# Kernel tuning notes

Hardware: AMD Instinct MI355X
Metric: run time of the kernel (lower is better)

The kernel has to match this reference:

```python
import jax, jax.numpy as jnp
import numpy as np

N = 100000   # nodes
E = 1600000  # edges (no self loops; module adds them)
D = 128      # in_dim == out_dim
BN_EPS = 1e-5
NORM_EPS = 1e-12


def setup_inputs() -> dict:
    key = jax.random.key(0)
    ks = jax.random.split(key, 9)
    x = jax.random.normal(ks[0], (N, D), jnp.float32)
    src = jax.random.randint(ks[1], (E,), 0, N, dtype=jnp.int32)
    dst = jax.random.randint(ks[2], (E,), 0, N, dtype=jnp.int32)
    dst = jnp.where(dst == src, (dst + 1) % N, dst)  # no pre-existing self loops
    edge_index = jnp.stack([src, dst], axis=0)
    edge_w = jax.random.uniform(ks[3], (E, 2), jnp.float32)
    # MySAGEConv.linear: Linear(2*D -> D) since concat=True
    W_lin = jax.random.normal(ks[4], (2 * D, D), jnp.float32) * (1.0 / np.sqrt(2 * D))
    b_lin = jnp.zeros((D,), jnp.float32)
    # BatchNorm1d(D)
    gamma = jnp.ones((D,), jnp.float32)
    beta = jnp.zeros((D,), jnp.float32)
    # PositionEmbedding(2, D): Linear(2->D//2, no bias), ReLU, Linear(D//2->D, no bias)
    pos_w1 = jax.random.normal(ks[5], (2, D // 2), jnp.float32) * 0.1
    pos_w2 = jax.random.normal(ks[6], (D // 2, D), jnp.float32) * 0.1
    return {"x": x, "edge_index": edge_index, "edge_w": edge_w,
            "W_lin": W_lin, "b_lin": b_lin, "gamma": gamma, "beta": beta,
            "pos_w1": pos_w1, "pos_w2": pos_w2}


def reference(x, edge_index, edge_w, W_lin, b_lin, gamma, beta, pos_w1, pos_w2):
    src, dst = edge_index[0], edge_index[1]
    # Position embedding is computed by the block but DISCARDED inside MySAGEConv.forward,
    # because add_remaining_self_loops(edge_index, None, 1, N) overwrites edge_weight with None.
    _pe = jnp.maximum(edge_w @ pos_w1, 0.0) @ pos_w2  # [E, D], unused (faithful to bug)
    # add_remaining_self_loops: append a self loop for every node
    loops = jnp.arange(N, dtype=src.dtype)
    src_f = jnp.concatenate([src, loops])
    dst_f = jnp.concatenate([dst, loops])
    # message = x_j (edge_weight is None); aggr = 'mean' scatter over destinations
    msg = x[src_f]                                           # [E+N, D] gather
    summed = jax.ops.segment_sum(msg, dst_f, num_segments=N)  # [N, D] scatter-add
    cnt = jax.ops.segment_sum(jnp.ones((E + N, 1), x.dtype), dst_f, num_segments=N)
    aggr = summed / cnt                                      # every node has >=1 (self loop)
    # update: concat + linear + L2 normalize
    h = jnp.concatenate([x, aggr], axis=-1) @ W_lin + b_lin   # [N, D]
    h = h / jnp.maximum(jnp.linalg.norm(h, axis=-1, keepdims=True), NORM_EPS)
    # BatchNorm1d (training-mode batch stats, biased variance)
    mu = jnp.mean(h, axis=0)
    var = jnp.var(h, axis=0)
    h = (h - mu) * jax.lax.rsqrt(var + BN_EPS) * gamma + beta
    # residual (in_dim == out_dim) + ReLU
    return jnp.maximum(h + x, 0.0)
```

## Files before the change

kernel.cpp:

```cpp
#include <hip/hip_runtime.h>
#include <hip/hip_bf16.h>

typedef __attribute__((ext_vector_type(4))) float f32x4;
typedef __attribute__((ext_vector_type(8))) short short8;
typedef unsigned short u16;
typedef unsigned long long u64;

#define NSLICE 64
#define LDSN 12544

static __device__ __forceinline__ u16 f2bf(float f) {
    __hip_bfloat16 h = __float2bfloat16(f);
    return __builtin_bit_cast(u16, h);
}
static __device__ __forceinline__ float bf2f(u16 u) {
    unsigned int w = ((unsigned int)u) << 16;
    return __builtin_bit_cast(float, w);
}

__global__ void k_pre(const float* __restrict__ x, u16* __restrict__ xb, int total8,
                      const int* __restrict__ dst, int* __restrict__ part,
                      int E, int chunk, int n, int cvtBlocks, int sl4) {
    __shared__ int lh[LDSN];
    int tid = threadIdx.x;
    if ((int)blockIdx.x < cvtBlocks) {
        const float4* x4 = (const float4*)x;
        int stride = cvtBlocks * 256;
        for (int i = blockIdx.x * 256 + tid; i < total8; i += stride) {
            float4 a = x4[i * 2], b = x4[i * 2 + 1];
            union { u16 u[8]; short8 v; } o;
            o.u[0] = f2bf(a.x); o.u[1] = f2bf(a.y); o.u[2] = f2bf(a.z); o.u[3] = f2bf(a.w);
            o.u[4] = f2bf(b.x); o.u[5] = f2bf(b.y); o.u[6] = f2bf(b.z); o.u[7] = f2bf(b.w);
            *(short8*)(xb + (size_t)i * 8) = o.v;
        }
    } else {
        int b = blockIdx.x - cvtBlocks;
        int g = b & 7;
        int s = b >> 3;
        int lo = g * chunk;
        int hi = min(lo + chunk, n);
        int cnt = hi - lo;
        for (int i = tid; i < cnt; i += 256) lh[i] = 0;
        __syncthreads();
        int E4 = E >> 2;
        const int4* d4 = (const int4*)dst;
        int i40 = s * sl4, i41 = min(i40 + sl4, E4);
        for (int i = i40 + tid; i < i41; i += 256) {
            int4 v = d4[i];
            if (v.x >= lo && v.x < hi) atomicAdd(&lh[v.x - lo], 1);
            if (v.y >= lo && v.y < hi) atomicAdd(&lh[v.y - lo], 1);
            if (v.z >= lo && v.z < hi) atomicAdd(&lh[v.z - lo], 1);
            if (v.w >= lo && v.w < hi) atomicAdd(&lh[v.w - lo], 1);
        }
        if (s == NSLICE - 1) {
            for (int e = E4 * 4 + tid; e < E; e += 256) {
                int d = dst[e];
                if (d >= lo && d < hi) atomicAdd(&lh[d - lo], 1);
            }
        }
        __syncthreads();
        int* pp = part + (size_t)s * n + lo;
        for (int i = tid; i < cnt; i += 256) pp[i] = lh[i];
    }
}

__global__ void k_scan_a(int* __restrict__ part, int* __restrict__ deg,
                         int* __restrict__ bsum, int n) {
    __shared__ int sm[256];
    int tid = threadIdx.x;
    int i = blockIdx.x * 256 + tid;
    int tot = 0;
    if (i < n) {
        int run = 0;
#pragma unroll
        for (int s = 0; s < NSLICE; ++s) {
            size_t idx = (size_t)s * n + i;
            int t = part[idx];
            part[idx] = run;
            run += t;
        }
        tot = run;
        deg[i] = run;
    }
    sm[tid] = tot;
    __syncthreads();
    for (int ofs = 128; ofs > 0; ofs >>= 1) {
        if (tid < ofs) sm[tid] += sm[tid + ofs];
        __syncthreads();
    }
    if (tid == 0) bsum[blockIdx.x] = sm[0];
}

__global__ void k_scan_b(const int* __restrict__ bsum, int* __restrict__ boff, int nb,
                         int* __restrict__ offN) {
    __shared__ int s[512];
    int tid = threadIdx.x;
    int v = (tid < nb) ? bsum[tid] : 0;
    s[tid] = v;
    __syncthreads();
    for (int ofs = 1; ofs < 512; ofs <<= 1) {
        int t = (tid >= ofs) ? s[tid - ofs] : 0;
        __syncthreads();
        s[tid] += t;
        __syncthreads();
    }
    if (tid < nb) boff[tid] = s[tid] - v;
    if (tid == nb - 1) offN[0] = s[tid];
}

__global__ void k_scan_c(const int* __restrict__ deg, const int* __restrict__ boff,
                         int* __restrict__ off, int n) {
    __shared__ int s[256];
    int tid = threadIdx.x;
    int i = blockIdx.x * 256 + tid;
    int v = (i < n) ? deg[i] : 0;
    s[tid] = v;
    __syncthreads();
    for (int ofs = 1; ofs < 256; ofs <<= 1) {
        int t = (tid >= ofs) ? s[tid - ofs] : 0;
        __syncthreads();
        s[tid] += t;
        __syncthreads();
    }
    int excl = s[tid] - v + boff[blockIdx.x];
    if (i < n) off[i] = excl;
}

__global__ void k_fill(const int* __restrict__ src, const int* __restrict__ dst,
                       const int* __restrict__ off, const int* __restrict__ pre,
                       int* __restrict__ csr, int E, int chunk, int n, int sl4) {
    __shared__ int lcnt[LDSN];
    int tid = threadIdx.x;
    int g = blockIdx.x & 7;
    int s = blockIdx.x >> 3;
    int lo = g * chunk;
    int hi = min(lo + chunk, n);
    int cnt = hi - lo;
    for (int i = tid; i < cnt; i += 256) lcnt[i] = 0;
    __syncthreads();
    int E4 = E >> 2;
    const int4* d4 = (const int4*)dst;
    const int4* s4 = (const int4*)src;
    const int* prs = pre + (size_t)s * n;
    int i40 = s * sl4, i41 = min(i40 + sl4, E4);
    for (int i = i40 + tid; i < i41; i += 256) {
        int4 v = d4[i];
        int4 u = s4[i];
        if (v.x >= lo && v.x < hi) {
            int p = off[v.x] + prs[v.x] + atomicAdd(&lcnt[v.x - lo], 1);
            csr[p] = u.x;
        }
        if (v.y >= lo && v.y < hi) {
            int p = off[v.y] + prs[v.y] + atomicAdd(&lcnt[v.y - lo], 1);
            csr[p] = u.y;
        }
        if (v.z >= lo && v.z < hi) {
            int p = off[v.z] + prs[v.z] + atomicAdd(&lcnt[v.z - lo], 1);
            csr[p] = u.z;
        }
        if (v.w >= lo && v.w < hi) {
            int p = off[v.w] + prs[v.w] + atomicAdd(&lcnt[v.w - lo], 1);
            csr[p] = u.w;
        }
    }
    if (s == NSLICE - 1) {
        for (int e = E4 * 4 + tid; e < E; e += 256) {
            int d = dst[e];
            if (d >= lo && d < hi) {
                int p = off[d] + prs[d] + atomicAdd(&lcnt[d - lo], 1);
                csr[p] = src[e];
            }
        }
    }
}

__global__ void k_aggr(const u16* __restrict__ xb, const int* __restrict__ off,
                       const int* __restrict__ csr, u16* __restrict__ aggr, int n) {
    int node = (blockIdx.x * blockDim.x + threadIdx.x) >> 6;
    if (node >= n) return;
    int lane = threadIdx.x & 63;
    int c = lane & 15;
    int j = lane >> 4;
    const short8* x8 = (const short8*)xb;
    int s0 = off[node], s1 = off[node + 1];
    float acc[8] = {0.f, 0.f, 0.f, 0.f, 0.f, 0.f, 0.f, 0.f};
    int e = s0;
    for (; e + 16 <= s1; e += 16) {
        int r0 = csr[e + j], r1 = csr[e + j + 4], r2 = csr[e + j + 8], r3 = csr[e + j + 12];
        short8 v0 = x8[(size_t)r0 * 16 + c];
        short8 v1 = x8[(size_t)r1 * 16 + c];
        short8 v2 = x8[(size_t)r2 * 16 + c];
        short8 v3 = x8[(size_t)r3 * 16 + c];
#pragma unroll
        for (int i = 0; i < 8; ++i)
            acc[i] += (bf2f((u16)v0[i]) + bf2f((u16)v1[i])) +
                      (bf2f((u16)v2[i]) + bf2f((u16)v3[i]));
    }
    for (int r = e + j; r < s1; r += 4) {
        short8 v = x8[(size_t)csr[r] * 16 + c];
#pragma unroll
        for (int i = 0; i < 8; ++i) acc[i] += bf2f((u16)v[i]);
    }
#pragma unroll
    for (int i = 0; i < 8; ++i) {
        acc[i] += __shfl_xor(acc[i], 16, 64);
        acc[i] += __shfl_xor(acc[i], 32, 64);
    }
    if (j == 0) {
        short8 sv = x8[(size_t)node * 16 + c];
        float inv = 1.0f / (float)(s1 - s0 + 1);
        short8 o;
#pragma unroll
        for (int i = 0; i < 8; ++i)
            o[i] = (short)f2bf((acc[i] + bf2f((u16)sv[i])) * inv);
        *(short8*)(aggr + (size_t)node * 128 + c * 8) = o;
    }
}

__global__ __launch_bounds__(512, 2) void k_linear(
    const float* __restrict__ x, const u16* __restrict__ aggr,
    const float* __restrict__ W, const float* __restrict__ b_lin,
    u16* __restrict__ hout ,
    float* __restrict__ ssp, float* __restrict__ bnsum, float* __restrict__ bnsq,
    int n, int ntiles, int npad) {
    __shared__ u16 WT[32768];
    int tid = threadIdx.x;

    {
        int col = tid & 127;
        int kq0 = tid >> 7;
        int mask = (col & 15) << 3;
        char* base = (char*)WT + col * 512;
#pragma unroll
        for (int i = 0; i < 16; ++i) {
            int kq = kq0 + i * 4;
            int k = kq * 4;
            float w0 = W[(size_t)(k + 0) * 128 + col];
            float w1 = W[(size_t)(k + 1) * 128 + col];
            float w2 = W[(size_t)(k + 2) * 128 + col];
            float w3 = W[(size_t)(k + 3) * 128 + col];
            u64 q = (u64)f2bf(w0) | ((u64)f2bf(w1) << 16) |
                    ((u64)f2bf(w2) << 32) | ((u64)f2bf(w3) << 48);
            *(u64*)(base + ((8 * kq) ^ mask)) = q;
        }
    }
    __syncthreads();

    int wave = tid >> 6, l = tid & 63, lr = l & 15, lg = l >> 4;
    int pair = wave >> 1, hf = wave & 1;

    short8 breg[4][8];
#pragma unroll
    for (int ct2 = 0; ct2 < 4; ++ct2) {
        int col = hf * 64 + ct2 * 16 + lr;
        const char* rowp = (const char*)WT + col * 512;
        int mask = (col & 15) << 3;
#pragma unroll
        for (int kk = 0; kk < 8; ++kk) {
            int kb = kk * 64 + 8 * lg;
            u64 lo = *(const u64*)(rowp + (kb ^ mask));
            u64 hi = *(const u64*)(rowp + ((kb + 32) ^ mask));
            union { u64 q[2]; short8 v; } bu;
            bu.q[0] = lo; bu.q[1] = hi;
            breg[ct2][kk] = bu.v;
        }
    }

    int stride4 = gridDim.x * 4;

    for (int base = blockIdx.x * 4; base < ntiles; base += stride4) {
        int tile = base + pair;
        bool active = tile < ntiles;
        int rowA = tile * 16 + lr;
        bool rv = active && rowA < n;

        float4 xa[4], xc[4];
        ushort4 ua[4], ub[4];
#pragma unroll
        for (int kk = 0; kk < 4; ++kk) {
            int k1 = kk * 32 + 4 * lg;
            xa[kk] = rv ? *(const float4*)(x + (size_t)rowA * 128 + k1)
                        : make_float4(0.f, 0.f, 0.f, 0.f);
            xc[kk] = rv ? *(const float4*)(x + (size_t)rowA * 128 + k1 + 16)
                        : make_float4(0.f, 0.f, 0.f, 0.f);
        }
#pragma unroll
        for (int kk = 0; kk < 4; ++kk) {
            const u16* ap = aggr + (size_t)rowA * 128 + kk * 32 + 4 * lg;
            ua[kk] = rv ? *(const ushort4*)ap : make_ushort4(0, 0, 0, 0);
            ub[kk] = rv ? *(const ushort4*)(ap + 16) : make_ushort4(0, 0, 0, 0);
        }

        short8 av[8];
#pragma unroll
        for (int kk = 0; kk < 4; ++kk) {
            av[kk][0] = (short)f2bf(xa[kk].x); av[kk][1] = (short)f2bf(xa[kk].y);
            av[kk][2] = (short)f2bf(xa[kk].z); av[kk][3] = (short)f2bf(xa[kk].w);
            av[kk][4] = (short)f2bf(xc[kk].x); av[kk][5] = (short)f2bf(xc[kk].y);
            av[kk][6] = (short)f2bf(xc[kk].z); av[kk][7] = (short)f2bf(xc[kk].w);
            av[kk + 4][0] = (short)ua[kk].x; av[kk + 4][1] = (short)ua[kk].y;
            av[kk + 4][2] = (short)ua[kk].z; av[kk + 4][3] = (short)ua[kk].w;
            av[kk + 4][4] = (short)ub[kk].x; av[kk + 4][5] = (short)ub[kk].y;
            av[kk + 4][6] = (short)ub[kk].z; av[kk + 4][7] = (short)ub[kk].w;
        }

        f32x4 acc[4];
#pragma unroll
        for (int ct2 = 0; ct2 < 4; ++ct2) acc[ct2] = (f32x4){0.f, 0.f, 0.f, 0.f};
#pragma unroll
        for (int kk = 0; kk < 8; ++kk)
#pragma unroll
            for (int ct2 = 0; ct2 < 4; ++ct2)
                acc[ct2] = __builtin_amdgcn_mfma_f32_16x16x32_bf16(av[kk], breg[ct2][kk],
                                                                   acc[ct2], 0, 0, 0);

        float ss[4] = {0.f, 0.f, 0.f, 0.f};
#pragma unroll
        for (int ct2 = 0; ct2 < 4; ++ct2) {
            float bl = b_lin[hf * 64 + ct2 * 16 + lr];
#pragma unroll
            for (int q = 0; q < 4; ++q) {
                acc[ct2][q] += bl;
                ss[q] += acc[ct2][q] * acc[ct2][q];
            }
        }
#pragma unroll
        for (int m = 1; m < 16; m <<= 1) {
#pragma unroll
            for (int q = 0; q < 4; ++q) ss[q] += __shfl_xor(ss[q], m, 64);
        }
        if (active) {
            int rq0 = tile * 16 + 4 * lg;
            if (lr == 0)
                *(float4*)&ssp[hf * npad + rq0] = make_float4(ss[0], ss[1], ss[2], ss[3]);
            u16* hp = hout + (size_t)tile * 4096 + 2048;
#pragma unroll
            for (int ct2 = 0; ct2 < 4; ++ct2) {
                ushort4 o;
                o.x = f2bf(acc[ct2][0]); o.y = f2bf(acc[ct2][1]);
                o.z = f2bf(acc[ct2][2]); o.w = f2bf(acc[ct2][3]);
                *(ushort4*)(hp + (hf * 4 + ct2) * 256 + l * 4) = o;
            }
        }
    }

    __syncthreads();

    float s1a[4] = {0, 0, 0, 0};
    float s2a[4] = {0, 0, 0, 0};
    for (int base = blockIdx.x * 4; base < ntiles; base += stride4) {
        int tile = base + pair;
        if (tile >= ntiles) continue;
        int rq0 = tile * 16 + 4 * lg;
        float rn[4];
#pragma unroll
        for (int q = 0; q < 4; ++q) {
            float s2 = ssp[rq0 + q] + ssp[npad + rq0 + q];
            rn[q] = 1.0f / fmaxf(sqrtf(s2), 1e-12f);
        }
        const u16* hp = hout + (size_t)tile * 4096 + 2048;
#pragma unroll
        for (int ct2 = 0; ct2 < 4; ++ct2) {
            ushort4 hv = *(const ushort4*)(hp + (hf * 4 + ct2) * 256 + l * 4);
            float p1 = 0.f, p2 = 0.f;
            float h0 = bf2f(hv.x) * rn[0], h1 = bf2f(hv.y) * rn[1];
            float h2 = bf2f(hv.z) * rn[2], h3 = bf2f(hv.w) * rn[3];
            if (rq0 + 0 < n) { p1 += h0; p2 += h0 * h0; }
            if (rq0 + 1 < n) { p1 += h1; p2 += h1 * h1; }
            if (rq0 + 2 < n) { p1 += h2; p2 += h2 * h2; }
            if (rq0 + 3 < n) { p1 += h3; p2 += h3 * h3; }
            s1a[ct2] += p1; s2a[ct2] += p2;
        }
    }

#pragma unroll
    for (int ct2 = 0; ct2 < 4; ++ct2) {
        float v1 = s1a[ct2], v2 = s2a[ct2];
        v1 += __shfl_xor(v1, 16, 64); v1 += __shfl_xor(v1, 32, 64);
        v2 += __shfl_xor(v2, 16, 64); v2 += __shfl_xor(v2, 32, 64);
        if (lg == 0) {
            atomicAdd(&bnsum[hf * 64 + ct2 * 16 + lr], v1);
            atomicAdd(&bnsq[hf * 64 + ct2 * 16 + lr], v2);
        }
    }
}

__global__ __launch_bounds__(512) void k_final(
    const float* __restrict__ ssp, const float* __restrict__ x,
    const float* __restrict__ bnsum, const float* __restrict__ bnsq,
    const float* __restrict__ gamma, const float* __restrict__ beta,
    float* __restrict__ out, float invN, int n, int npad) {
    __shared__ float cf[256];
    __shared__ float ot[16 * 132];
    int tid = threadIdx.x;
    int tile = blockIdx.x;
    if (tid < 128) {
        float mu = bnsum[tid] * invN;
        float var = bnsq[tid] * invN - mu * mu;
        float a = gamma[tid] * rsqrtf(var + 1e-5f);
        cf[tid] = a;
        cf[128 + tid] = beta[tid] - mu * a;
    }
    __syncthreads();

    {
        const u16* hp = (const u16*)out + (size_t)tile * 4096 + 2048;
        int ct = tid >> 6, l = tid & 63;
        ushort4 hv = *(const ushort4*)(hp + ct * 256 + l * 4);
        int col = ct * 16 + (l & 15);
        float a = cf[col], b = cf[128 + col];
        int rl0 = 4 * (l >> 4);
        int rq0 = tile * 16 + rl0;
        float rn0 = 1.0f / fmaxf(sqrtf(ssp[rq0 + 0] + ssp[npad + rq0 + 0]), 1e-12f);
        float rn1 = 1.0f / fmaxf(sqrtf(ssp[rq0 + 1] + ssp[npad + rq0 + 1]), 1e-12f);
        float rn2 = 1.0f / fmaxf(sqrtf(ssp[rq0 + 2] + ssp[npad + rq0 + 2]), 1e-12f);
        float rn3 = 1.0f / fmaxf(sqrtf(ssp[rq0 + 3] + ssp[npad + rq0 + 3]), 1e-12f);
        ot[(rl0 + 0) * 132 + col] = bf2f(hv.x) * rn0 * a + b;
        ot[(rl0 + 1) * 132 + col] = bf2f(hv.y) * rn1 * a + b;
        ot[(rl0 + 2) * 132 + col] = bf2f(hv.z) * rn2 * a + b;
        ot[(rl0 + 3) * 132 + col] = bf2f(hv.w) * rn3 * a + b;
    }
    __syncthreads();

    {
        int rl = tid >> 5, c4 = tid & 31;
        int row = tile * 16 + rl;
        if (row < n) {
            float4 xv = *(const float4*)(x + (size_t)row * 128 + c4 * 4);
            const float* op = &ot[rl * 132 + c4 * 4];
            float4 o;
            o.x = fmaxf(op[0] + xv.x, 0.f);
            o.y = fmaxf(op[1] + xv.y, 0.f);
            o.z = fmaxf(op[2] + xv.z, 0.f);
            o.w = fmaxf(op[3] + xv.w, 0.f);
            *(float4*)(out + (size_t)row * 128 + c4 * 4) = o;
        }
    }
}

extern "C" void kernel_launch(void* const* d_in, const int* in_sizes, int n_in,
                              void* d_out, int out_size, void* d_ws, size_t ws_size,
                              hipStream_t stream) {
    const float* x     = (const float*)d_in[0];
    const int*   ei    = (const int*)d_in[1];
    const float* W     = (const float*)d_in[3];
    const float* b_lin = (const float*)d_in[4];
    const float* gamma = (const float*)d_in[5];
    const float* beta  = (const float*)d_in[6];
    int N = in_sizes[0] / 128;
    int E = in_sizes[1] / 2;
    const int* src = ei;
    const int* dst = ei + E;

    int ntiles = (N + 15) / 16;
    int npad = ntiles * 16;

    char* p = (char*)d_ws;
    auto alloc = [&](size_t bytes) { char* r = p; p += (bytes + 255) & ~(size_t)255; return r; };
    int*   deg   = (int*)alloc((size_t)N * 4);
    float* bnsum = (float*)alloc(128 * 4);
    float* bnsq  = (float*)alloc(128 * 4);
    size_t zoff  = (char*)bnsum - (char*)d_ws;
    int*   off   = (int*)alloc((size_t)(N + 1) * 4);
    int*   csr   = (int*)alloc((size_t)E * 4);
    int*   bsum  = (int*)alloc(512 * 4);
    int*   boff  = (int*)alloc(512 * 4);
    float* ssp   = (float*)alloc((size_t)npad * 2 * 4);
    u16*   aggr  = (u16*)alloc((size_t)N * 128 * 2);

    int* part = (int*)aggr;

    u16* xbf = (u16*)d_out;

    hipMemsetAsync((char*)d_ws + zoff, 0, 256 * 4, stream);

    int chunk = (N + 7) / 8;
    int E4 = E >> 2;
    int sl4 = (E4 + NSLICE - 1) / NSLICE;
    const int CVTB = 768;

    k_pre<<<CVTB + 8 * NSLICE, 256, 0, stream>>>(x, xbf, N * 16, dst, part,
                                                 E, chunk, N, CVTB, sl4);
    int nb = (N + 255) / 256;
    k_scan_a<<<nb, 256, 0, stream>>>(part, deg, bsum, N);
    k_scan_b<<<1, 512, 0, stream>>>(bsum, boff, nb, off + N);
    k_scan_c<<<nb, 256, 0, stream>>>(deg, boff, off, N);
    k_fill<<<8 * NSLICE, 256, 0, stream>>>(src, dst, off, part, csr, E, chunk, N, sl4);
    k_aggr<<<(int)(((size_t)N * 64 + 255) / 256), 256, 0, stream>>>(xbf, off, csr, aggr, N);
    k_linear<<<512, 512, 0, stream>>>(x, aggr, W, b_lin, (u16*)d_out, ssp,
                                      bnsum, bnsq, N, ntiles, npad);
    k_final<<<ntiles, 512, 0, stream>>>(ssp, x, bnsum, bnsq, gamma, beta,
                                        (float*)d_out, 1.0f / (float)N, N, npad);
}
```

Before: 269.3 us.

## Feed linear kernel with bf16 x, separate h buffer, halve slices and grid

k_linear now reads the bf16 copy of x already produced by k_pre instead of fp32 x, which halves that input traffic and removes the conversions. Its pre-normalisation output goes to a dedicated workspace buffer instead of the upper half of the output array, because xbf also lives in d_out and would otherwise be clobbered. The edge-slice count for the CSR build drops from 64 to 32 and the linear grid from 512 to 256 blocks, which changes parallelism and per-block work. This adds an extra workspace allocation.

```diff
diff --git a/kernel.cpp b/kernel.cpp
--- a/kernel.cpp
+++ b/kernel.cpp
@@ -6,7 +6,7 @@
 typedef unsigned short u16;
 typedef unsigned long long u64;
 
-#define NSLICE 64
+#define NSLICE 32
 #define LDSN 12544
 
 static __device__ __forceinline__ u16 f2bf(float f) {
@@ -218,9 +218,9 @@
 }
 
 __global__ __launch_bounds__(512, 2) void k_linear(
-    const float* __restrict__ x, const u16* __restrict__ aggr,
+    const u16* __restrict__ xb, const u16* __restrict__ aggr,
     const float* __restrict__ W, const float* __restrict__ b_lin,
-    u16* __restrict__ hout ,
+    u16* __restrict__ hfrag,
     float* __restrict__ ssp, float* __restrict__ bnsum, float* __restrict__ bnsq,
     int n, int ntiles, int npad) {
     __shared__ u16 WT[32768];
@@ -274,15 +274,12 @@
         int rowA = tile * 16 + lr;
         bool rv = active && rowA < n;
 
-        float4 xa[4], xc[4];
-        ushort4 ua[4], ub[4];
+        ushort4 xba[4], xbb[4], ua[4], ub[4];
 #pragma unroll
         for (int kk = 0; kk < 4; ++kk) {
-            int k1 = kk * 32 + 4 * lg;
-            xa[kk] = rv ? *(const float4*)(x + (size_t)rowA * 128 + k1)
-                        : make_float4(0.f, 0.f, 0.f, 0.f);
-            xc[kk] = rv ? *(const float4*)(x + (size_t)rowA * 128 + k1 + 16)
-                        : make_float4(0.f, 0.f, 0.f, 0.f);
+            const u16* xp = xb + (size_t)rowA * 128 + kk * 32 + 4 * lg;
+            xba[kk] = rv ? *(const ushort4*)xp : make_ushort4(0, 0, 0, 0);
+            xbb[kk] = rv ? *(const ushort4*)(xp + 16) : make_ushort4(0, 0, 0, 0);
         }
 #pragma unroll
         for (int kk = 0; kk < 4; ++kk) {
@@ -294,10 +291,10 @@
         short8 av[8];
 #pragma unroll
         for (int kk = 0; kk < 4; ++kk) {
-            av[kk][0] = (short)f2bf(xa[kk].x); av[kk][1] = (short)f2bf(xa[kk].y);
-            av[kk][2] = (short)f2bf(xa[kk].z); av[kk][3] = (short)f2bf(xa[kk].w);
-            av[kk][4] = (short)f2bf(xc[kk].x); av[kk][5] = (short)f2bf(xc[kk].y);
-            av[kk][6] = (short)f2bf(xc[kk].z); av[kk][7] = (short)f2bf(xc[kk].w);
+            av[kk][0] = (short)xba[kk].x; av[kk][1] = (short)xba[kk].y;
+            av[kk][2] = (short)xba[kk].z; av[kk][3] = (short)xba[kk].w;
+            av[kk][4] = (short)xbb[kk].x; av[kk][5] = (short)xbb[kk].y;
+            av[kk][6] = (short)xbb[kk].z; av[kk][7] = (short)xbb[kk].w;
             av[kk + 4][0] = (short)ua[kk].x; av[kk + 4][1] = (short)ua[kk].y;
             av[kk + 4][2] = (short)ua[kk].z; av[kk + 4][3] = (short)ua[kk].w;
             av[kk + 4][4] = (short)ub[kk].x; av[kk + 4][5] = (short)ub[kk].y;
@@ -333,7 +330,7 @@
             int rq0 = tile * 16 + 4 * lg;
             if (lr == 0)
                 *(float4*)&ssp[hf * npad + rq0] = make_float4(ss[0], ss[1], ss[2], ss[3]);
-            u16* hp = hout + (size_t)tile * 4096 + 2048;
+            u16* hp = hfrag + (size_t)tile * 2048;
 #pragma unroll
             for (int ct2 = 0; ct2 < 4; ++ct2) {
                 ushort4 o;
@@ -358,7 +355,7 @@
             float s2 = ssp[rq0 + q] + ssp[npad + rq0 + q];
             rn[q] = 1.0f / fmaxf(sqrtf(s2), 1e-12f);
         }
-        const u16* hp = hout + (size_t)tile * 4096 + 2048;
+        const u16* hp = hfrag + (size_t)tile * 2048;
 #pragma unroll
         for (int ct2 = 0; ct2 < 4; ++ct2) {
             ushort4 hv = *(const ushort4*)(hp + (hf * 4 + ct2) * 256 + l * 4);
@@ -386,6 +383,7 @@
 }
 
 __global__ __launch_bounds__(512) void k_final(
+    const u16* __restrict__ hfrag,
     const float* __restrict__ ssp, const float* __restrict__ x,
     const float* __restrict__ bnsum, const float* __restrict__ bnsq,
     const float* __restrict__ gamma, const float* __restrict__ beta,
@@ -404,7 +402,7 @@
     __syncthreads();
 
     {
-        const u16* hp = (const u16*)out + (size_t)tile * 4096 + 2048;
+        const u16* hp = hfrag + (size_t)tile * 2048;
         int ct = tid >> 6, l = tid & 63;
         ushort4 hv = *(const ushort4*)(hp + ct * 256 + l * 4);
         int col = ct * 16 + (l & 15);
@@ -467,6 +465,7 @@
     int*   boff  = (int*)alloc(512 * 4);
     float* ssp   = (float*)alloc((size_t)npad * 2 * 4);
     u16*   aggr  = (u16*)alloc((size_t)N * 128 * 2);
+    u16*   hfrag = (u16*)alloc((size_t)npad * 128 * 2);
 
     int* part = (int*)aggr;
 
@@ -487,8 +486,8 @@
     k_scan_c<<<nb, 256, 0, stream>>>(deg, boff, off, N);
     k_fill<<<8 * NSLICE, 256, 0, stream>>>(src, dst, off, part, csr, E, chunk, N, sl4);
     k_aggr<<<(int)(((size_t)N * 64 + 255) / 256), 256, 0, stream>>>(xbf, off, csr, aggr, N);
-    k_linear<<<512, 512, 0, stream>>>(x, aggr, W, b_lin, (u16*)d_out, ssp,
+    k_linear<<<256, 512, 0, stream>>>(xbf, aggr, W, b_lin, hfrag, ssp,
                                       bnsum, bnsq, N, ntiles, npad);
-    k_final<<<ntiles, 512, 0, stream>>>(ssp, x, bnsum, bnsq, gamma, beta,
+    k_final<<<ntiles, 512, 0, stream>>>(hfrag, ssp, x, bnsum, bnsq, gamma, beta,
                                         (float*)d_out, 1.0f / (float)N, N, npad);
 }
```

Measured after the change: 282.0 us. 1.05x slower.
